# Kernel optimization log

Measured on AMD Instinct MI355X. Metric: run time of the kernel, lower is better.

## Reference

```python
import jax, jax.numpy as jnp
import numpy as np

EPS = 1e-9


def _approx_match(xyz1, xyz2):
    """Faithful reimplementation of Fan et al. approxmatch CUDA kernel.

    xyz1: (b, n, 3), xyz2: (b, m, 3)
    Returns (match (b,n,m), sqdist (b,n,m)).
    """
    b, n, _ = xyz1.shape
    m = xyz2.shape[1]
    # pairwise squared distances (b, n, m)
    d2 = jnp.sum((xyz1[:, :, None, :] - xyz2[:, None, :, :]) ** 2, axis=-1)
    mx = float(max(n, m))
    remainL = jnp.full((b, n), mx / n, dtype=xyz1.dtype)  # mass left on xyz1 side
    remainR = jnp.full((b, m), mx / m, dtype=xyz1.dtype)  # mass left on xyz2 side
    match = jnp.zeros((b, n, m), dtype=xyz1.dtype)
    # annealing schedule: level = -4^j for j = 7..-1, then level = 0
    for j in range(7, -3, -1):
        level = 0.0 if j == -2 else -(4.0 ** j)
        w = jnp.exp(level * d2) * remainR[:, None, :]                    # (b,n,m)
        w = w / (jnp.sum(w, axis=2, keepdims=True) + EPS) * remainL[:, :, None]
        sumr = jnp.sum(w, axis=1)                                        # (b,m)
        cons = jnp.minimum(remainR / (sumr + EPS), 1.0)                  # column saturation
        w = w * cons[:, None, :]
        match = match + w
        remainL = jnp.maximum(remainL - jnp.sum(w, axis=2), 0.0)
        remainR = jnp.maximum(remainR - sumr * cons, 0.0)
    return match, d2


def setup_inputs() -> dict:
    key = jax.random.key(0)
    k1, k2 = jax.random.split(key)
    xyz1 = jax.random.normal(k1, (16, 2048, 3), dtype=jnp.float32)
    xyz2 = jax.random.normal(k2, (16, 2048, 3), dtype=jnp.float32)
    return {"xyz1": xyz1, "xyz2": xyz2}


def reference(xyz1, xyz2):
    # matchcost_forward: cost_b = sum_{i,l} match[i,l] * ||x1_i - x2_l||
    match, d2 = _approx_match(xyz1, xyz2)
    return jnp.sum(match * jnp.sqrt(d2), axis=(1, 2))  # (b,)
```

## Files before the change

kernel.cpp:

```cpp
#include <hip/hip_runtime.h>

#define BB 16
#define NN 2048
#define MM 2048
#define EPSF 1e-9f
#define SKIPT (-135.0f)

typedef float v2f __attribute__((ext_vector_type(2)));

constexpr int CH = 64;

__global__ __launch_bounds__(256) void init_kernel(
    const float* __restrict__ xyz1, const float* __restrict__ xyz2,
    float4* __restrict__ P1, float4* __restrict__ P2,
    float* __restrict__ remR0,
    float* __restrict__ stRS, float* __restrict__ stU,
    float* __restrict__ stS, float* __restrict__ stT,
    float* __restrict__ out)
{
    const int t = blockIdx.x * 256 + threadIdx.x;
    if (t < BB * NN) {
        P1[t] = make_float4(xyz1[3*t+0], xyz1[3*t+1], xyz1[3*t+2], 0.0f);
        stRS[t] = 0.0f; stRS[BB*NN + t] = 0.0f;
        stU[t]  = 0.0f; stU[BB*NN + t]  = 0.0f;
    }
    if (t < BB * MM) {
        P2[t] = make_float4(xyz2[3*t+0], xyz2[3*t+1], xyz2[3*t+2], 0.0f);
        remR0[t] = 1.0f;
        stS[t] = 0.0f; stS[BB*MM + t] = 0.0f;
        stT[t] = 0.0f; stT[BB*MM + t] = 0.0f;
    }
    if (t < BB) out[t] = 0.0f;
}

__global__ __launch_bounds__(256) void rowInit(
    const float4* __restrict__ P1, const float4* __restrict__ P2,
    float* __restrict__ stRSacc, float coef)
{
    __shared__ float4 sCol[CH];
    const int chunks = MM / CH;
    const int bpb = (NN / 512) * chunks;
    const int batch = blockIdx.x / bpb;
    const int rem   = blockIdx.x % bpb;
    const int rg    = rem / chunks;
    const int ic    = rem % chunks;
    const int t     = threadIdx.x;

    if (t < CH) sCol[t] = P2[batch * MM + ic * CH + t];
    __syncthreads();

    const int row0 = batch * NN + rg * 512 + t;
    const int row1 = row0 + 256;
    const float4 p0 = P1[row0];
    const float4 p1 = P1[row1];
    const v2f px = {p0.x, p1.x}, py = {p0.y, p1.y}, pz = {p0.z, p1.z};
    v2f rs = {0.0f, 0.0f};
#pragma unroll 4
    for (int ii = 0; ii < CH; ++ii) {
        const float4 q = sCol[ii];
        const v2f dx = px - q.x, dy = py - q.y, dz = pz - q.z;
        const v2f g = coef * (dx*dx + dy*dy + dz*dz);
        if (__ballot((g.x > SKIPT) || (g.y > SKIPT))) {
            v2f e;
            e.x = __builtin_amdgcn_exp2f(g.x);
            e.y = __builtin_amdgcn_exp2f(g.y);
            rs += e;
        }
    }
    atomicAdd(&stRSacc[row0], rs.x);
    atomicAdd(&stRSacc[row1], rs.y);
}

template<int MODE, bool SPARSE>
__global__ __launch_bounds__(256) void colK(
    const float4* __restrict__ P1, const float4* __restrict__ P2,
    const float* __restrict__ stRSr, const float* __restrict__ stUr,
    float* __restrict__ stRSz, float* __restrict__ stUz,
    const float* __restrict__ remLr, float* __restrict__ remLw,
    const float* __restrict__ scaler, float* __restrict__ scalew,
    float* __restrict__ stS, float* __restrict__ stT,
    float coef)
{
    __shared__ float4 sRow[CH];
    const int chunks = NN / CH;
    const int bpb = (MM / 512) * chunks;
    const int batch = blockIdx.x / bpb;
    const int rem   = blockIdx.x % bpb;
    const int cg    = rem / chunks;
    const int ic    = rem % chunks;
    const int t     = threadIdx.x;

    if (t < CH) {
        const int gi = batch * NN + ic * CH + t;
        float L;
        if (MODE == 0) L = 1.0f;
        else           L = fmaxf(remLr[gi] - scaler[gi] * stUr[gi], 0.0f);
        remLw[gi] = L;
        const float sc = L / (stRSr[gi] + EPSF);
        scalew[gi] = sc;
        const float4 p = P1[gi];
        sRow[t] = make_float4(p.x, p.y, p.z, sc);
        stRSz[gi] = 0.0f; stUz[gi] = 0.0f;
    }
    __syncthreads();

    const int col0 = batch * MM + cg * 512 + t;
    const int col1 = col0 + 256;
    const float4 q0 = P2[col0];
    const float4 q1 = P2[col1];
    const v2f qx = {q0.x, q1.x}, qy = {q0.y, q1.y}, qz = {q0.z, q1.z};
    v2f s = {0.0f, 0.0f}, tt = {0.0f, 0.0f};
#pragma unroll 4
    for (int ii = 0; ii < CH; ++ii) {
        const float4 a = sRow[ii];
        const v2f dx = a.x - qx, dy = a.y - qy, dz = a.z - qz;
        const v2f d2 = dx*dx + dy*dy + dz*dz;
        if (SPARSE) {
            const v2f g = coef * d2;
            if (__ballot((g.x > SKIPT) || (g.y > SKIPT))) {
                v2f e;
                e.x = __builtin_amdgcn_exp2f(g.x);
                e.y = __builtin_amdgcn_exp2f(g.y);
                e *= a.w;
                v2f sq;
                sq.x = __builtin_amdgcn_sqrtf(d2.x);
                sq.y = __builtin_amdgcn_sqrtf(d2.y);
                s += e;
                tt += e * sq;
            }
        } else {
            v2f e;
            if (MODE == 2) { e.x = a.w; e.y = a.w; }
            else {
                const v2f g = coef * d2;
                e.x = a.w * __builtin_amdgcn_exp2f(g.x);
                e.y = a.w * __builtin_amdgcn_exp2f(g.y);
            }
            v2f sq;
            sq.x = __builtin_amdgcn_sqrtf(d2.x);
            sq.y = __builtin_amdgcn_sqrtf(d2.y);
            s += e;
            tt += e * sq;
        }
    }
    atomicAdd(&stS[col0], s.x);
    atomicAdd(&stT[col0], tt.x);
    atomicAdd(&stS[col1], s.y);
    atomicAdd(&stT[col1], tt.y);
}

template<int MODE, bool SPARSE>
__global__ __launch_bounds__(256) void rowK(
    const float4* __restrict__ P1, const float4* __restrict__ P2,
    const float* __restrict__ stSr, const float* __restrict__ stTr,
    float* __restrict__ stSz, float* __restrict__ stTz,
    const float* __restrict__ remRr, float* __restrict__ remRw,
    float* __restrict__ stRS, float* __restrict__ stU,
    float* __restrict__ out,
    float coefP, float coefN)
{
    __shared__ float4 sCol[CH];
    __shared__ float  sPc[CH];
    const int chunks = MM / CH;
    const int bpb = (NN / 512) * chunks;
    const int batch = blockIdx.x / bpb;
    const int rem   = blockIdx.x % bpb;
    const int rg    = rem / chunks;
    const int ic    = rem % chunks;
    const int t     = threadIdx.x;

    float c = 0.0f;
    if (t < CH) {
        const int gl = batch * MM + ic * CH + t;
        const float R  = remRr[gl];
        const float s  = stSr[gl];
        const float t2 = stTr[gl];
        const float sumr = s * R;
        const float cons = fminf(R / (sumr + EPSF), 1.0f);
        const float pcol = R * cons;
        const float Rn   = fmaxf(R - sumr * cons, 0.0f);
        remRw[gl] = Rn;
        const float4 p = P2[gl];
        sCol[t] = make_float4(p.x, p.y, p.z, Rn);
        sPc[t]  = pcol;
        stSz[gl] = 0.0f; stTz[gl] = 0.0f;
        if (rg == 0) c = pcol * t2;
    }
    if (rg == 0) {
#pragma unroll
        for (int off = 32; off > 0; off >>= 1) c += __shfl_xor(c, off, 64);
        if (t < CH && (t & 63) == 0) atomicAdd(out + batch, c);
    }
    __syncthreads();

    const int row0 = batch * NN + rg * 512 + t;
    const int row1 = row0 + 256;
    const float4 p0 = P1[row0];
    const float4 p1 = P1[row1];
    const v2f px = {p0.x, p1.x}, py = {p0.y, p1.y}, pz = {p0.z, p1.z};
    v2f rs = {0.0f, 0.0f}, u = {0.0f, 0.0f};
#pragma unroll 4
    for (int ii = 0; ii < CH; ++ii) {
        const float4 q = sCol[ii];
        const float pc = sPc[ii];
        const v2f dx = px - q.x, dy = py - q.y, dz = pz - q.z;
        const v2f d2 = dx*dx + dy*dy + dz*dz;
        if (MODE == 1) {
            const v2f g = coefN * d2;
            if (SPARSE) {
                if (__ballot((g.x > SKIPT) || (g.y > SKIPT))) {
                    v2f en;
                    en.x = __builtin_amdgcn_exp2f(g.x);
                    en.y = __builtin_amdgcn_exp2f(g.y);
                    const v2f e2 = en * en;
                    const v2f e4 = e2 * e2;
                    u  += e4 * pc;
                    rs += en * q.w;
                }
            } else {
                v2f en;
                en.x = __builtin_amdgcn_exp2f(g.x);
                en.y = __builtin_amdgcn_exp2f(g.y);
                const v2f e2 = en * en;
                const v2f e4 = e2 * e2;
                u  += e4 * pc;
                rs += en * q.w;
            }
        } else {
            const v2f g = coefP * d2;
            v2f ep;
            ep.x = __builtin_amdgcn_exp2f(g.x);
            ep.y = __builtin_amdgcn_exp2f(g.y);
            u  += ep * pc;
            rs += q.w;
        }
    }
    atomicAdd(&stRS[row0], rs.x);
    atomicAdd(&stU[row0], u.x);
    atomicAdd(&stRS[row1], rs.y);
    atomicAdd(&stU[row1], u.y);
}

__global__ __launch_bounds__(256) void finCost(
    const float* __restrict__ stSr, const float* __restrict__ stTr,
    const float* __restrict__ remRr, float* __restrict__ out)
{
    const int idx = blockIdx.x * 256 + threadIdx.x;
    const int batch = idx / MM;
    const float R = remRr[idx];
    const float sumr = stSr[idx] * R;
    const float cons = fminf(R / (sumr + EPSF), 1.0f);
    float c = R * cons * stTr[idx];
#pragma unroll
    for (int off = 32; off > 0; off >>= 1) c += __shfl_xor(c, off, 64);
    if ((threadIdx.x & 63) == 0) atomicAdd(out + batch, c);
}

extern "C" void kernel_launch(void* const* d_in, const int* in_sizes, int n_in,
                              void* d_out, int out_size, void* d_ws, size_t ws_size,
                              hipStream_t stream)
{
    const float* xyz1 = (const float*)d_in[0];
    const float* xyz2 = (const float*)d_in[1];
    float* out = (float*)d_out;

    const int BN = BB * NN, BM = BB * MM;
    float4* P1 = (float4*)d_ws;
    float4* P2 = P1 + BN;
    float* remL  = (float*)(P2 + BM);
    float* scale = remL + 2 * BN;
    float* remR  = scale + 2 * BN;
    float* stRS  = remR + 2 * BM;
    float* stU   = stRS + 2 * BN;
    float* stS   = stU + 2 * BN;
    float* stT   = stS + 2 * BM;

    init_kernel<<<dim3(BN / 256), dim3(256), 0, stream>>>(
        xyz1, xyz2, P1, P2, remR, stRS, stU, stS, stT, out);

    float coef[10];
    const double lv[10] = {-16384.0, -4096.0, -1024.0, -256.0, -64.0,
                           -16.0, -4.0, -1.0, -0.25, 0.0};
    for (int i = 0; i < 10; ++i) coef[i] = (float)(lv[i] * 1.4426950408889634);

    dim3 grid(BB * 4 * (NN / CH));
    dim3 fgrid(BM / 256);
    dim3 blk(256);

    rowInit<<<grid, blk, 0, stream>>>(P1, P2, stRS + 1 * BN, coef[0]);

    for (int j = 0; j < 10; ++j) {
        const int p = j & 1, q = 1 - p;
        if (j == 0)
            colK<0, true><<<grid, blk, 0, stream>>>(P1, P2,
                stRS + q*BN, stU + q*BN, stRS + p*BN, stU + p*BN,
                remL + p*BN, remL + q*BN, scale + p*BN, scale + q*BN,
                stS + p*BM, stT + p*BM, coef[0]);
        else if (j <= 3)
            colK<1, true><<<grid, blk, 0, stream>>>(P1, P2,
                stRS + q*BN, stU + q*BN, stRS + p*BN, stU + p*BN,
                remL + p*BN, remL + q*BN, scale + p*BN, scale + q*BN,
                stS + p*BM, stT + p*BM, coef[j]);
        else if (j == 9)
            colK<2, false><<<grid, blk, 0, stream>>>(P1, P2,
                stRS + q*BN, stU + q*BN, stRS + p*BN, stU + p*BN,
                remL + p*BN, remL + q*BN, scale + p*BN, scale + q*BN,
                stS + p*BM, stT + p*BM, coef[9]);
        else
            colK<1, false><<<grid, blk, 0, stream>>>(P1, P2,
                stRS + q*BN, stU + q*BN, stRS + p*BN, stU + p*BN,
                remL + p*BN, remL + q*BN, scale + p*BN, scale + q*BN,
                stS + p*BM, stT + p*BM, coef[j]);

        if (j < 9) {
            if (j <= 2)
                rowK<1, true><<<grid, blk, 0, stream>>>(P1, P2,
                    stS + p*BM, stT + p*BM, stS + q*BM, stT + q*BM,
                    remR + p*BM, remR + q*BM,
                    stRS + p*BN, stU + p*BN, out, coef[j], coef[j+1]);
            else if (j < 8)
                rowK<1, false><<<grid, blk, 0, stream>>>(P1, P2,
                    stS + p*BM, stT + p*BM, stS + q*BM, stT + q*BM,
                    remR + p*BM, remR + q*BM,
                    stRS + p*BN, stU + p*BN, out, coef[j], coef[j+1]);
            else
                rowK<2, false><<<grid, blk, 0, stream>>>(P1, P2,
                    stS + p*BM, stT + p*BM, stS + q*BM, stT + q*BM,
                    remR + p*BM, remR + q*BM,
                    stRS + p*BN, stU + p*BN, out, coef[8], 0.0f);
        }
    }
    finCost<<<fgrid, blk, 0, stream>>>(stS + 1*BM, stT + 1*BM, remR + 1*BM, out);
}
```

Measured before the change: 515.7 us.

## Morton-sort points per batch to enable tile skipping in more annealing levels

Adds a per-batch kernel that sorts both point clouds along a Morton curve using a shared-memory bitonic sort, so nearby points land in the same tiles. With spatially coherent tiles, the skip-enabled (bounding-threshold) variants of the row and column kernels are used for more annealing levels (up to level 5/4 instead of 3/2). The cost is assumed invariant to point order since it sums over all pairs. Risks: the added sort launch, and whether the skip threshold remains accurate at weaker levels.

Result: slower. 554.2 us (+7.5%).

```diff
diff --git a/kernel.cpp b/kernel.cpp
--- a/kernel.cpp
+++ b/kernel.cpp
@@ -31,6 +31,59 @@
         stT[t] = 0.0f; stT[BB*MM + t] = 0.0f;
     }
     if (t < BB) out[t] = 0.0f;
+}
+
+__device__ inline unsigned mortonExpand(unsigned v) {
+    v = (v | (v << 16)) & 0x030000FFu;
+    v = (v | (v << 8))  & 0x0300F00Fu;
+    v = (v | (v << 4))  & 0x030C30C3u;
+    v = (v | (v << 2))  & 0x09249249u;
+    return v;
+}
+
+__global__ __launch_bounds__(1024) void sortK(float4* __restrict__ P1,
+                                              float4* __restrict__ P2)
+{
+    __shared__ unsigned long long keys[2048];
+    __shared__ float4 pts[2048];
+    const int batch = blockIdx.x & 15;
+    float4* P = (blockIdx.x >> 4) ? (P2 + batch * MM) : (P1 + batch * NN);
+    const int tid = threadIdx.x;
+
+#pragma unroll
+    for (int r = 0; r < 2; ++r) {
+        const int i = tid + r * 1024;
+        const float4 p = P[i];
+        pts[i] = p;
+        const unsigned qx = (unsigned)fminf(fmaxf((p.x + 4.0f) * 128.0f, 0.0f), 1023.0f);
+        const unsigned qy = (unsigned)fminf(fmaxf((p.y + 4.0f) * 128.0f, 0.0f), 1023.0f);
+        const unsigned qz = (unsigned)fminf(fmaxf((p.z + 4.0f) * 128.0f, 0.0f), 1023.0f);
+        const unsigned code = mortonExpand(qx) | (mortonExpand(qy) << 1)
+                            | (mortonExpand(qz) << 2);
+        keys[i] = ((unsigned long long)code << 32) | (unsigned)i;
+    }
+
+    for (int k = 2; k <= 2048; k <<= 1) {
+        for (int j = k >> 1; j > 0; j >>= 1) {
+            __syncthreads();
+#pragma unroll
+            for (int r = 0; r < 2; ++r) {
+                const int i = tid + r * 1024;
+                const int ixj = i ^ j;
+                if (ixj > i) {
+                    const bool up = ((i & k) == 0);
+                    const unsigned long long a = keys[i], b = keys[ixj];
+                    if ((a > b) == up) { keys[i] = b; keys[ixj] = a; }
+                }
+            }
+        }
+    }
+    __syncthreads();
+#pragma unroll
+    for (int r = 0; r < 2; ++r) {
+        const int i = tid + r * 1024;
+        P[i] = pts[(unsigned)keys[i]];
+    }
 }
 
 __global__ __launch_bounds__(256) void rowInit(
@@ -278,6 +331,8 @@
     init_kernel<<<dim3(BN / 256), dim3(256), 0, stream>>>(
         xyz1, xyz2, P1, P2, remR, stRS, stU, stS, stT, out);
 
+    sortK<<<dim3(32), dim3(1024), 0, stream>>>(P1, P2);
+
     float coef[10];
     const double lv[10] = {-16384.0, -4096.0, -1024.0, -256.0, -64.0,
                            -16.0, -4.0, -1.0, -0.25, 0.0};
@@ -296,7 +351,7 @@
                 stRS + q*BN, stU + q*BN, stRS + p*BN, stU + p*BN,
                 remL + p*BN, remL + q*BN, scale + p*BN, scale + q*BN,
                 stS + p*BM, stT + p*BM, coef[0]);
-        else if (j <= 3)
+        else if (j <= 5)
             colK<1, true><<<grid, blk, 0, stream>>>(P1, P2,
                 stRS + q*BN, stU + q*BN, stRS + p*BN, stU + p*BN,
                 remL + p*BN, remL + q*BN, scale + p*BN, scale + q*BN,
@@ -313,7 +368,7 @@
                 stS + p*BM, stT + p*BM, coef[j]);
 
         if (j < 9) {
-            if (j <= 2)
+            if (j <= 4)
                 rowK<1, true><<<grid, blk, 0, stream>>>(P1, P2,
                     stS + p*BM, stT + p*BM, stS + q*BM, stT + q*BM,
                     remR + p*BM, remR + q*BM,
```
